# Kernel tuning notes

Hardware: AMD Instinct MI355X
Metric: run time of the kernel (lower is better)

The kernel has to match this reference:

```python
import jax, jax.numpy as jnp
import numpy as np

T, H = 4096, 2048  # seq_len, hidden/feature size (hidden == features per module code)

def setup_inputs() -> dict:
    key = jax.random.key(0)
    k1, k2, k3 = jax.random.split(key, 3)
    s = 1.0 / np.sqrt(H).astype(np.float32)
    return {
        "x": jax.random.normal(k1, (T, H), jnp.float32),
        "c0": jnp.zeros((H,), jnp.float32),
        "h0": jnp.zeros((H,), jnp.float32),
        "Wi": jax.random.normal(k2, (H, 4 * H), jnp.float32) * s,  # input kernel, gates [i,f,g,o]
        "Wh": jax.random.normal(k3, (H, 4 * H), jnp.float32) * s,  # recurrent kernel
        "b": jnp.zeros((4 * H,), jnp.float32),
    }

def reference(x, c0, h0, Wi, Wh, b):
    # Faithful to flax.linen.OptimizedLSTMCell scanned over time (gate order i,f,g,o).
    def step(carry, xt):
        c, h = carry
        y = xt @ Wi + h @ Wh + b          # (4H,)
        i, f, g, o = jnp.split(y, 4)
        i = jax.nn.sigmoid(i)
        f = jax.nn.sigmoid(f)
        g = jnp.tanh(g)
        o = jax.nn.sigmoid(o)
        c_new = f * c + i * g
        h_new = o * jnp.tanh(c_new)
        return (c_new, h_new), h_new

    (c_f, h_f), ys = jax.lax.scan(step, (c0, h0), x)
    return c_f, h_f, ys
```

## Files before the change

kernel.cpp:

```cpp
#include <hip/hip_runtime.h>
#include <math.h>

#define T_STEPS 4096
#define HDIM    2048
#define KDIM    2048
#define NG      8192
#define CTR_STRIDE 16
#define NREC    2048

typedef unsigned long long ull;

__global__ void init_ws4(const float* __restrict__ h0,
                         unsigned* __restrict__ ctr,
                         uint2* __restrict__ recs) {
    int g = blockIdx.x * blockDim.x + threadIdx.x;
    if (g < 8 * CTR_STRIDE) ctr[g] = ((g % CTR_STRIDE) == 0) ? 32u : 0u;
    int d = g - 8 * CTR_STRIDE;
    if (d >= 0 && d < 2 * NREC) {
        int slot = d >> 11;
        int r = d & (NREC - 1);
        uint2 v;
        if (slot == 1) {
            v.x = __float_as_uint(h0[r]);
            v.y = 0u;
        } else {
            v.x = 0u;
            v.y = 0xFFFFFFFFu;
        }
        recs[d] = v;
    }
}

__global__ __launch_bounds__(256) void gemm_xwi(
    const float* __restrict__ X, const float* __restrict__ Wi,
    const float* __restrict__ bias, float* __restrict__ Y)
{
    __shared__ float As[16][65];
    __shared__ __align__(16) float Bs[16][64];
    const int tid = threadIdx.x;
    const int m0 = blockIdx.y * 64;
    const int n0 = blockIdx.x * 64;
    const int tx4 = (tid & 15) * 4;
    const int ty4 = (tid >> 4) * 4;
    const int am = tid >> 2, ak = (tid & 3) * 4;
    const int bk = tid >> 4, bn = (tid & 15) * 4;

    float acc[4][4];
#pragma unroll
    for (int i = 0; i < 4; ++i)
#pragma unroll
        for (int j = 0; j < 4; ++j) acc[i][j] = 0.f;

    for (int kt = 0; kt < KDIM; kt += 16) {
        float4 av = *reinterpret_cast<const float4*>(&X[(size_t)(m0 + am) * KDIM + kt + ak]);
        float4 bv = *reinterpret_cast<const float4*>(&Wi[(size_t)(kt + bk) * NG + n0 + bn]);
        __syncthreads();
        As[ak + 0][am] = av.x; As[ak + 1][am] = av.y;
        As[ak + 2][am] = av.z; As[ak + 3][am] = av.w;
        *reinterpret_cast<float4*>(&Bs[bk][bn]) = bv;
        __syncthreads();
#pragma unroll
        for (int k = 0; k < 16; ++k) {
            float a0 = As[k][ty4 + 0], a1 = As[k][ty4 + 1];
            float a2 = As[k][ty4 + 2], a3 = As[k][ty4 + 3];
            float4 b4 = *reinterpret_cast<const float4*>(&Bs[k][tx4]);
            acc[0][0] = fmaf(a0, b4.x, acc[0][0]); acc[0][1] = fmaf(a0, b4.y, acc[0][1]);
            acc[0][2] = fmaf(a0, b4.z, acc[0][2]); acc[0][3] = fmaf(a0, b4.w, acc[0][3]);
            acc[1][0] = fmaf(a1, b4.x, acc[1][0]); acc[1][1] = fmaf(a1, b4.y, acc[1][1]);
            acc[1][2] = fmaf(a1, b4.z, acc[1][2]); acc[1][3] = fmaf(a1, b4.w, acc[1][3]);
            acc[2][0] = fmaf(a2, b4.x, acc[2][0]); acc[2][1] = fmaf(a2, b4.y, acc[2][1]);
            acc[2][2] = fmaf(a2, b4.z, acc[2][2]); acc[2][3] = fmaf(a2, b4.w, acc[2][3]);
            acc[3][0] = fmaf(a3, b4.x, acc[3][0]); acc[3][1] = fmaf(a3, b4.y, acc[3][1]);
            acc[3][2] = fmaf(a3, b4.z, acc[3][2]); acc[3][3] = fmaf(a3, b4.w, acc[3][3]);
        }
    }
    float4 bb = *reinterpret_cast<const float4*>(&bias[n0 + tx4]);
#pragma unroll
    for (int i = 0; i < 4; ++i) {
        float4 o;
        o.x = acc[i][0] + bb.x; o.y = acc[i][1] + bb.y;
        o.z = acc[i][2] + bb.z; o.w = acc[i][3] + bb.w;
        *reinterpret_cast<float4*>(&Y[(size_t)(m0 + ty4 + i) * NG + n0 + tx4]) = o;
    }
}

__device__ __forceinline__ float fsigm(float x) { return 1.f / (1.f + __expf(-x)); }
__device__ __forceinline__ float ftanh(float x) {
    float ax = fabsf(x);
    float e  = __expf(2.f * ax);
    float t  = (e - 1.f) / (e + 1.f);
    t = (ax > 15.f) ? 1.f : t;
    return copysignf(t, x);
}

__global__ __launch_bounds__(512)
__attribute__((amdgpu_waves_per_eu(2, 2)))
void lstm_persistent(
    const float* __restrict__ Y,
    const float* __restrict__ c0,
    const float* __restrict__ Wh,
    uint2* __restrict__ recs,
    unsigned* __restrict__ ctr,
    float* __restrict__ out)
{
    const int b    = blockIdx.x;
    const int tid  = threadIdx.x;
    const int lane = tid & 63;
    const int w    = tid >> 6;
    const int gg   = w >> 1;
    const int hg   = w & 1;
    const int nbase = (gg << 11) + (b << 3) + (hg << 2);

    __shared__ __align__(16) float hlds[HDIM];
    __shared__ float gates[32];
    __shared__ float c_s[8];
    __shared__ float hlast[8];
    __shared__ unsigned ldsflag;

    float4 wreg[32];
#pragma unroll
    for (int j = 0; j < 8; ++j)
#pragma unroll
        for (int m = 0; m < 4; ++m) {
            const size_t k = (size_t)(4 * lane + 256 * j + m);
            wreg[j * 4 + m] = *reinterpret_cast<const float4*>(&Wh[k * NG + nbase]);
        }
#pragma unroll
    for (int i = 0; i < 32; ++i) {
        asm volatile("" : "+v"(wreg[i].x), "+v"(wreg[i].y),
                          "+v"(wreg[i].z), "+v"(wreg[i].w));
    }

    if (tid < 8) c_s[tid] = c0[b * 8 + tid];
    if (tid == 0) ldsflag = 0xFFFFFFFFu;
    __syncthreads();

    for (int t = 0; t < T_STEPS; ++t) {
        const int rs = (t + 1) & 1;
        const unsigned target = 32u * (unsigned)(t + 1);

        float yv = 0.f;
        if (lane < 4) yv = Y[(size_t)t * NG + nbase + lane];

        if (w == 0) {
            const unsigned* cp = ctr + (size_t)(lane & 7) * CTR_STRIDE;
            for (;;) {
                unsigned v = target;
                if (lane < 8)
                    v = __hip_atomic_load(cp, __ATOMIC_RELAXED, __HIP_MEMORY_SCOPE_SYSTEM);
                if (__all(v >= target)) break;
                __builtin_amdgcn_s_sleep(1);
            }
            if (lane == 0)
                __hip_atomic_store(&ldsflag, (unsigned)t, __ATOMIC_RELEASE,
                                   __HIP_MEMORY_SCOPE_WORKGROUP);
        } else {
            while (__hip_atomic_load(&ldsflag, __ATOMIC_ACQUIRE,
                                     __HIP_MEMORY_SCOPE_WORKGROUP) != (unsigned)t)
                __builtin_amdgcn_s_sleep(1);
        }

        {
            const uint2* rb = recs + (size_t)rs * NREC;
            const uint2* p0 = rb + 2 * tid;
            const uint2* p1 = rb + 1024 + 2 * tid;
            const unsigned expt = (unsigned)t;
            uint4 ra, rc;
            for (;;) {
                asm volatile("global_load_dwordx4 %0, %2, off sc0 sc1\n\t"
                             "global_load_dwordx4 %1, %3, off sc0 sc1\n\t"
                             "s_waitcnt vmcnt(0)"
                             : "=&v"(ra), "=&v"(rc)
                             : "v"(p0), "v"(p1) : "memory");
                if (__all((ra.y == expt) & (ra.w == expt) &
                          (rc.y == expt) & (rc.w == expt))) break;
                __builtin_amdgcn_s_sleep(1);
            }
            float2 d0; d0.x = __uint_as_float(ra.x); d0.y = __uint_as_float(ra.z);
            float2 d1; d1.x = __uint_as_float(rc.x); d1.y = __uint_as_float(rc.z);
            *reinterpret_cast<float2*>(&hlds[2 * tid])        = d0;
            *reinterpret_cast<float2*>(&hlds[1024 + 2 * tid]) = d1;
        }
        __syncthreads();

        float4 acc; acc.x = acc.y = acc.z = acc.w = 0.f;
#pragma unroll
        for (int j = 0; j < 8; ++j) {
            float4 h4 = reinterpret_cast<const float4*>(hlds)[lane + 64 * j];
            float4 w0 = wreg[4 * j + 0], w1 = wreg[4 * j + 1];
            float4 w2 = wreg[4 * j + 2], w3 = wreg[4 * j + 3];
            acc.x = fmaf(h4.x, w0.x, acc.x); acc.x = fmaf(h4.y, w1.x, acc.x);
            acc.x = fmaf(h4.z, w2.x, acc.x); acc.x = fmaf(h4.w, w3.x, acc.x);
            acc.y = fmaf(h4.x, w0.y, acc.y); acc.y = fmaf(h4.y, w1.y, acc.y);
            acc.y = fmaf(h4.z, w2.y, acc.y); acc.y = fmaf(h4.w, w3.y, acc.y);
            acc.z = fmaf(h4.x, w0.z, acc.z); acc.z = fmaf(h4.y, w1.z, acc.z);
            acc.z = fmaf(h4.z, w2.z, acc.z); acc.z = fmaf(h4.w, w3.z, acc.z);
            acc.w = fmaf(h4.x, w0.w, acc.w); acc.w = fmaf(h4.y, w1.w, acc.w);
            acc.w = fmaf(h4.z, w2.w, acc.w); acc.w = fmaf(h4.w, w3.w, acc.w);
        }
#pragma unroll
        for (int off = 32; off >= 1; off >>= 1) {
            acc.x += __shfl_xor(acc.x, off);
            acc.y += __shfl_xor(acc.y, off);
            acc.z += __shfl_xor(acc.z, off);
            acc.w += __shfl_xor(acc.w, off);
        }
        if (lane < 4) {
            float v = (lane == 0) ? acc.x : (lane == 1) ? acc.y
                    : (lane == 2) ? acc.z : acc.w;
            gates[gg * 8 + hg * 4 + lane] = v + yv;
        }
        __syncthreads();

        if (tid < 8) {
            float iv = gates[0 * 8 + tid];
            float fv = gates[1 * 8 + tid];
            float gv = gates[2 * 8 + tid];
            float ov = gates[3 * 8 + tid];
            float cn = fsigm(fv) * c_s[tid] + fsigm(iv) * ftanh(gv);
            float hn = fsigm(ov) * ftanh(cn);
            c_s[tid] = cn;
            hlast[tid] = hn;
            ull rec = ((ull)(unsigned)(t + 1) << 32) | (ull)__float_as_uint(hn);
            uint2* dst = recs + (size_t)(t & 1) * NREC + b * 8 + tid;
            asm volatile("global_store_dwordx2 %0, %1, off sc0 sc1"
                         :: "v"(dst), "v"(rec) : "memory");
            if (tid == 0)
                __hip_atomic_fetch_add(ctr + (size_t)(b >> 5) * CTR_STRIDE, 1u,
                                       __ATOMIC_RELAXED, __HIP_MEMORY_SCOPE_SYSTEM);
            __builtin_nontemporal_store(hn, &out[2 * HDIM + (size_t)t * HDIM + b * 8 + tid]);
        }
    }

    if (tid < 8) {
        out[b * 8 + tid]        = c_s[tid];
        out[HDIM + b * 8 + tid] = hlast[tid];
    }
}

extern "C" void kernel_launch(void* const* d_in, const int* in_sizes, int n_in,
                              void* d_out, int out_size, void* d_ws, size_t ws_size,
                              hipStream_t stream) {
    const float* x   = (const float*)d_in[0];
    const float* c0  = (const float*)d_in[1];
    const float* h0  = (const float*)d_in[2];
    const float* Wi  = (const float*)d_in[3];
    const float* Wh  = (const float*)d_in[4];
    const float* bia = (const float*)d_in[5];
    float* out = (float*)d_out;

    char* base = (char*)d_ws;
    float* Y = (float*)base;
    base += (size_t)T_STEPS * NG * sizeof(float);
    unsigned* ctr = (unsigned*)base;
    base += 8 * CTR_STRIDE * sizeof(unsigned);
    uint2* recs = (uint2*)base;

    const int initN = 8 * CTR_STRIDE + 2 * NREC;
    hipLaunchKernelGGL(init_ws4, dim3((initN + 511) / 512), dim3(512), 0, stream,
                       h0, ctr, recs);
    hipLaunchKernelGGL(gemm_xwi, dim3(NG / 64, T_STEPS / 64), dim3(256), 0, stream,
                       x, Wi, bia, Y);

    void* args[] = { (void*)&Y, (void*)&c0, (void*)&Wh,
                     (void*)&recs, (void*)&ctr, (void*)&out };
    (void)hipLaunchCooperativeKernel((const void*)lstm_persistent, dim3(256), dim3(512),
                                     args, 0, stream);
}
```

Before: 13.86 ms.

## Replace counter barrier with triple-buffered tagged h records

Removes the global atomic step counters and the wave-0 spin plus LDS flag handoff. Blocks now sync only by polling the step-tagged h records, and the records use three rotating slots so a fast block cannot overwrite a slot a slow block is still reading. This drops an atomic round trip and an intra-block relay from the per-step critical path. In exchange, every thread spins on global record loads directly, which may add memory traffic while waiting.

```diff
diff --git a/kernel.cpp b/kernel.cpp
--- a/kernel.cpp
+++ b/kernel.cpp
@@ -5,22 +5,19 @@
 #define HDIM    2048
 #define KDIM    2048
 #define NG      8192
-#define CTR_STRIDE 16
 #define NREC    2048
+#define NSLOT   3
 
 typedef unsigned long long ull;
 
-__global__ void init_ws4(const float* __restrict__ h0,
-                         unsigned* __restrict__ ctr,
+__global__ void init_ws5(const float* __restrict__ h0,
                          uint2* __restrict__ recs) {
-    int g = blockIdx.x * blockDim.x + threadIdx.x;
-    if (g < 8 * CTR_STRIDE) ctr[g] = ((g % CTR_STRIDE) == 0) ? 32u : 0u;
-    int d = g - 8 * CTR_STRIDE;
-    if (d >= 0 && d < 2 * NREC) {
+    int d = blockIdx.x * blockDim.x + threadIdx.x;
+    if (d < NSLOT * NREC) {
         int slot = d >> 11;
         int r = d & (NREC - 1);
         uint2 v;
-        if (slot == 1) {
+        if (slot == 2) {
             v.x = __float_as_uint(h0[r]);
             v.y = 0u;
         } else {
@@ -100,7 +97,6 @@
     const float* __restrict__ c0,
     const float* __restrict__ Wh,
     uint2* __restrict__ recs,
-    unsigned* __restrict__ ctr,
     float* __restrict__ out)
 {
     const int b    = blockIdx.x;
@@ -115,7 +111,6 @@
     __shared__ float gates[32];
     __shared__ float c_s[8];
     __shared__ float hlast[8];
-    __shared__ unsigned ldsflag;
 
     float4 wreg[32];
 #pragma unroll
@@ -132,33 +127,14 @@
     }
 
     if (tid < 8) c_s[tid] = c0[b * 8 + tid];
-    if (tid == 0) ldsflag = 0xFFFFFFFFu;
     __syncthreads();
 
+    int rs = 2;
+    int ws = 0;
+
     for (int t = 0; t < T_STEPS; ++t) {
-        const int rs = (t + 1) & 1;
-        const unsigned target = 32u * (unsigned)(t + 1);
-
         float yv = 0.f;
         if (lane < 4) yv = Y[(size_t)t * NG + nbase + lane];
-
-        if (w == 0) {
-            const unsigned* cp = ctr + (size_t)(lane & 7) * CTR_STRIDE;
-            for (;;) {
-                unsigned v = target;
-                if (lane < 8)
-                    v = __hip_atomic_load(cp, __ATOMIC_RELAXED, __HIP_MEMORY_SCOPE_SYSTEM);
-                if (__all(v >= target)) break;
-                __builtin_amdgcn_s_sleep(1);
-            }
-            if (lane == 0)
-                __hip_atomic_store(&ldsflag, (unsigned)t, __ATOMIC_RELEASE,
-                                   __HIP_MEMORY_SCOPE_WORKGROUP);
-        } else {
-            while (__hip_atomic_load(&ldsflag, __ATOMIC_ACQUIRE,
-                                     __HIP_MEMORY_SCOPE_WORKGROUP) != (unsigned)t)
-                __builtin_amdgcn_s_sleep(1);
-        }
 
         {
             const uint2* rb = recs + (size_t)rs * NREC;
@@ -222,14 +198,14 @@
             c_s[tid] = cn;
             hlast[tid] = hn;
             ull rec = ((ull)(unsigned)(t + 1) << 32) | (ull)__float_as_uint(hn);
-            uint2* dst = recs + (size_t)(t & 1) * NREC + b * 8 + tid;
+            uint2* dst = recs + (size_t)ws * NREC + b * 8 + tid;
             asm volatile("global_store_dwordx2 %0, %1, off sc0 sc1"
                          :: "v"(dst), "v"(rec) : "memory");
-            if (tid == 0)
-                __hip_atomic_fetch_add(ctr + (size_t)(b >> 5) * CTR_STRIDE, 1u,
-                                       __ATOMIC_RELAXED, __HIP_MEMORY_SCOPE_SYSTEM);
             __builtin_nontemporal_store(hn, &out[2 * HDIM + (size_t)t * HDIM + b * 8 + tid]);
         }
+
+        rs = ws;
+        ws = (ws == 2) ? 0 : ws + 1;
     }
 
     if (tid < 8) {
@@ -252,18 +228,16 @@
     char* base = (char*)d_ws;
     float* Y = (float*)base;
     base += (size_t)T_STEPS * NG * sizeof(float);
-    unsigned* ctr = (unsigned*)base;
-    base += 8 * CTR_STRIDE * sizeof(unsigned);
     uint2* recs = (uint2*)base;
 
-    const int initN = 8 * CTR_STRIDE + 2 * NREC;
-    hipLaunchKernelGGL(init_ws4, dim3((initN + 511) / 512), dim3(512), 0, stream,
-                       h0, ctr, recs);
+    const int initN = NSLOT * NREC;
+    hipLaunchKernelGGL(init_ws5, dim3((initN + 511) / 512), dim3(512), 0, stream,
+                       h0, recs);
     hipLaunchKernelGGL(gemm_xwi, dim3(NG / 64, T_STEPS / 64), dim3(256), 0, stream,
                        x, Wi, bia, Y);
 
     void* args[] = { (void*)&Y, (void*)&c0, (void*)&Wh,
-                     (void*)&recs, (void*)&ctr, (void*)&out };
+                     (void*)&recs, (void*)&out };
     (void)hipLaunchCooperativeKernel((const void*)lstm_persistent, dim3(256), dim3(512),
                                      args, 0, stream);
 }
```

Result: no change. 13.92 ms (+0.4%).
